# Kernel tuning notes

Hardware: AMD Instinct MI355X
Metric: run time of the kernel (lower is better)

The kernel has to match this reference:

```python
import jax, jax.numpy as jnp
import numpy as np

TOP_K = 2
SMOOTHING = 0.9


def setup_inputs() -> dict:
    key = jax.random.key(0)
    k1, k2, k3 = jax.random.split(key, 3)
    T, D, E = 16384, 2048, 64
    x = jax.random.normal(k1, (T, D), dtype=jnp.float32)
    gate_w = jax.random.normal(k2, (D, E), dtype=jnp.float32) * (1.0 / np.sqrt(D))
    expert_loads = jax.random.uniform(k3, (E,), dtype=jnp.float32)
    expert_loads = expert_loads / jnp.sum(expert_loads)  # normalized load estimate
    return {"x": x, "gate_w": gate_w, "expert_loads": expert_loads}


def reference(x, gate_w, expert_loads):
    T, _ = x.shape
    E = gate_w.shape[1]
    # Gate projection: [T, D] @ [D, E] -> [T, E]
    logits = jnp.matmul(x, gate_w)
    # Load-balancing bias injection (ExpertLoadBalancer.get_balancing_biases):
    # bias = -(load - 1/E) * 2, added to logits for expert *selection* only.
    biases = -(expert_loads - 1.0 / E) * 2.0
    _, top_idx = jax.lax.top_k(logits + biases[None, :], TOP_K)  # [T, K] int32
    # Routing weights: softmax over the selected (unbiased) logits.
    top_logits = jnp.take_along_axis(logits, top_idx, axis=1)  # [T, K]
    routing_weights = jax.nn.softmax(top_logits, axis=-1)  # [T, K]
    # Vectorized load update (replaces the Python double loop in update_loads):
    # scatter-add routing weights per expert, normalize by token count, EMA-smooth.
    current_loads = jax.ops.segment_sum(
        routing_weights.reshape(-1), top_idx.reshape(-1), num_segments=E
    ) / T
    new_loads = SMOOTHING * expert_loads + (1.0 - SMOOTHING) * current_loads
    return routing_weights, top_idx, new_loads
```

## Files before the change

kernel.cpp:

```cpp
#include <hip/hip_runtime.h>

#define TT 16384
#define DD 2048
#define EE 64

typedef __attribute__((ext_vector_type(8))) short bf16x8;
typedef __attribute__((ext_vector_type(8))) unsigned short ushort8;
typedef __attribute__((ext_vector_type(4))) float f32x4;

__device__ __forceinline__ unsigned short bf16_rne(float f) {
    unsigned u = __float_as_uint(f);
    return (unsigned short)((u + 0x7FFFu + ((u >> 16) & 1u)) >> 16);
}
__device__ __forceinline__ float bf16_f32(unsigned short h) {
    return __uint_as_float(((unsigned)h) << 16);
}
__device__ __forceinline__ unsigned cvt_pk(float lo, float hi) {
    unsigned r;
    asm("v_cvt_pk_bf16_f32 %0, %1, %2" : "=v"(r) : "v"(lo), "v"(hi));
    return r;
}
__device__ __forceinline__ bf16x8 pack4(unsigned a, unsigned b, unsigned c, unsigned d) {
    union { unsigned u[4]; bf16x8 v; } t;
    t.u[0] = a; t.u[1] = b; t.u[2] = c; t.u[3] = d;
    return t.v;
}
__device__ __forceinline__ void gload16(void* lds, const void* g) {
    __builtin_amdgcn_global_load_lds(
        (const __attribute__((address_space(1))) unsigned int*)g,
        (__attribute__((address_space(3))) unsigned int*)lds, 16, 0, 0);
}

__global__ __launch_bounds__(256)
void wconv(const float* __restrict__ wg, unsigned short* __restrict__ wpack) {
    const int t = (int)blockIdx.x * 256 + threadIdx.x;
    const int K0 = t >> 9, h = (t >> 8) & 1, m = (t >> 6) & 3, lane = t & 63;
    const int e = m * 16 + (lane & 15);
    const int ks = K0 * 32 + (lane >> 4) * 8;
    ushort8 v;
#pragma unroll
    for (int j = 0; j < 8; ++j) {
        const float f = wg[(size_t)(ks + j) * EE + e];
        const unsigned short hi = bf16_rne(f);
        v[j] = h ? bf16_rne(f - bf16_f32(hi)) : hi;
    }
    *(ushort8*)(wpack + ((size_t)(K0 * 8 + h * 4 + m) * 64 + lane) * 8) = v;
}

__global__ __launch_bounds__(512, 4)
void gate_fused(const float* __restrict__ x, const unsigned short* __restrict__ wpack,
                const float* __restrict__ loads, float* __restrict__ out,
                float* __restrict__ binpart) {
    __shared__ __align__(16) float arena[3 * 4096];
    __shared__ float bins[2][64];

    const int tid = threadIdx.x, lane = tid & 63, w = tid >> 6;
    const int tg = w >> 2, q = w & 3;
    const int tb = (int)blockIdx.x;

    f32x4 acc[4] = {{0,0,0,0},{0,0,0,0},{0,0,0,0},{0,0,0,0}};

    auto stage_x = [&](int s, float* rb) {
#pragma unroll
        for (int i = 0; i < 2; ++i) {
            const int n = (w << 1) | i;
            const int qw = n >> 2, g = n & 3;
            const int rowp = lane >> 3;
            const int row = g * 8 + rowp;
            const int c = (lane & 7) ^ rowp;
            gload16(rb + qw * 1024 + g * 256,
                    x + (size_t)(tb * 32 + row) * DD + qw * 512 + s * 32 + c * 4);
        }
    };
    auto loadW = [&](int t, bf16x8 (&wh)[4], bf16x8 (&wl)[4]) {
        const unsigned short* base = wpack + (size_t)(q * 16 + t) * 4096 + lane * 8;
#pragma unroll
        for (int m = 0; m < 4; ++m) {
            wh[m] = *(const bf16x8*)(base + (size_t)m * 512);
            wl[m] = *(const bf16x8*)(base + (size_t)(4 + m) * 512);
        }
    };
    auto compute = [&](const float* rb, bf16x8 (&wh)[4], bf16x8 (&wl)[4]) {
        const float* xq = rb + q * 1024;
        const int row = tg * 16 + (lane & 15);
        const int kgc = (lane >> 4) << 1;
        const int sw = row & 7;
        const f32x4 va = *(const f32x4*)(xq + row * 32 + ((kgc) ^ sw) * 4);
        const f32x4 vb = *(const f32x4*)(xq + row * 32 + ((kgc + 1) ^ sw) * 4);
        const float cf[8] = {va.x, va.y, va.z, va.w, vb.x, vb.y, vb.z, vb.w};
        unsigned ph[4], pl[4];
#pragma unroll
        for (int j = 0; j < 4; ++j) {
            ph[j] = cvt_pk(cf[2 * j], cf[2 * j + 1]);
            const float h0 = __uint_as_float(ph[j] << 16);
            const float h1 = __uint_as_float(ph[j] & 0xFFFF0000u);
            pl[j] = cvt_pk(cf[2 * j] - h0, cf[2 * j + 1] - h1);
        }
        const bf16x8 bhi = pack4(ph[0], ph[1], ph[2], ph[3]);
        const bf16x8 blo = pack4(pl[0], pl[1], pl[2], pl[3]);
#pragma unroll
        for (int m = 0; m < 4; ++m) {
            acc[m] = __builtin_amdgcn_mfma_f32_16x16x32_bf16(wh[m], bhi, acc[m], 0, 0, 0);
            acc[m] = __builtin_amdgcn_mfma_f32_16x16x32_bf16(wh[m], blo, acc[m], 0, 0, 0);
            acc[m] = __builtin_amdgcn_mfma_f32_16x16x32_bf16(wl[m], bhi, acc[m], 0, 0, 0);
        }
    };

    float *p0 = arena, *p1 = arena + 4096, *p2 = arena + 8192;
    bf16x8 whA[4], wlA[4], whB[4], wlB[4];

    stage_x(0, p0);
    stage_x(1, p1);
    loadW(0, whA, wlA);
    asm volatile("s_waitcnt vmcnt(10)" ::: "memory");
    __builtin_amdgcn_s_barrier();

#pragma unroll 1
    for (int s = 0; s < 14; s += 2) {
        stage_x(s + 2, p2);
        loadW(s + 1, whB, wlB);
        compute(p0, whA, wlA);
        asm volatile("s_waitcnt vmcnt(10)" ::: "memory");
        __builtin_amdgcn_s_barrier();
        { float* t_ = p0; p0 = p1; p1 = p2; p2 = t_; }

        stage_x(s + 3, p2);
        loadW(s + 2, whA, wlA);
        compute(p0, whB, wlB);
        asm volatile("s_waitcnt vmcnt(10)" ::: "memory");
        __builtin_amdgcn_s_barrier();
        { float* t_ = p0; p0 = p1; p1 = p2; p2 = t_; }
    }
    loadW(15, whB, wlB);
    compute(p0, whA, wlA);
    asm volatile("s_waitcnt vmcnt(8)" ::: "memory");
    __builtin_amdgcn_s_barrier();
    compute(p1, whB, wlB);

    __syncthreads();
    float* accb = arena;
    if (q != 0) {
#pragma unroll
        for (int m = 0; m < 4; ++m)
            *(f32x4*)(accb + ((size_t)((q - 1) * 128 + tg * 64 + lane) * 20 + m * 4)) = acc[m];
    }
    __syncthreads();
    if (q != 0) return;

    f32x4 r[4];
#pragma unroll
    for (int m = 0; m < 4; ++m) {
        f32x4 s_ = acc[m];
#pragma unroll
        for (int qq = 0; qq < 3; ++qq) {
            const f32x4 t_ =
                *(const f32x4*)(accb + ((size_t)(qq * 128 + tg * 64 + lane) * 20 + m * 4));
            s_.x += t_.x; s_.y += t_.y; s_.z += t_.z; s_.w += t_.w;
        }
        r[m] = s_;
    }

    const int col = lane & 15;
    const int tok = tb * 32 + tg * 16 + col;
    const int erow = (lane >> 4) * 4;
    float v1 = -3.4e38f, u1 = 0.0f, v2 = -3.4e38f, u2 = 0.0f;
    int i1 = 0x7fffffff, i2 = 0x7fffffff;
#pragma unroll
    for (int m = 0; m < 4; ++m)
#pragma unroll
        for (int rr = 0; rr < 4; ++rr) {
            const int e = m * 16 + erow + rr;
            const float u = r[m][rr];
            const float b = u - (loads[e] - 0.015625f) * 2.0f;
            if ((b > v1) || (b == v1 && e < i1)) {
                v2 = v1; u2 = u1; i2 = i1;
                v1 = b;  u1 = u;  i1 = e;
            } else if ((b > v2) || (b == v2 && e < i2)) {
                v2 = b; u2 = u; i2 = e;
            }
        }
#pragma unroll
    for (int s = 0; s < 2; ++s) {
        const int mask = 16 << s;
        const float ov1 = __shfl_xor(v1, mask), ou1 = __shfl_xor(u1, mask);
        const float ov2 = __shfl_xor(v2, mask), ou2 = __shfl_xor(u2, mask);
        const int oi1 = __shfl_xor(i1, mask), oi2 = __shfl_xor(i2, mask);
        if ((ov1 > v1) || (ov1 == v1 && oi1 < i1)) {
            if ((v1 > ov2) || (v1 == ov2 && i1 < oi2)) { v2 = v1; u2 = u1; i2 = i1; }
            else                                        { v2 = ov2; u2 = ou2; i2 = oi2; }
            v1 = ov1; u1 = ou1; i1 = oi1;
        } else if ((ov1 > v2) || (ov1 == v2 && oi1 < i2)) {
            v2 = ov1; u2 = ou1; i2 = oi1;
        }
    }

    bins[tg][lane] = 0.0f;
    if (lane < 16) {
        const float mx = fmaxf(u1, u2);
        const float e1 = __expf(u1 - mx), e2 = __expf(u2 - mx);
        const float w1 = e1 / (e1 + e2), w2 = e2 / (e1 + e2);
        *(float2*)(out + 2 * tok) = make_float2(w1, w2);
        *(float2*)(out + 2 * TT + 2 * tok) = make_float2((float)i1, (float)i2);
        atomicAdd(&bins[tg][i1], w1);
        atomicAdd(&bins[tg][i2], w2);
    }
    binpart[(size_t)(tb * 2 + tg) * 64 + lane] = bins[tg][lane];
}

__global__ __launch_bounds__(256)
void finalize1(const float* __restrict__ binpart, float* __restrict__ binmid) {
    __shared__ float p[4][64];
    const int e = threadIdx.x & 63, sub = threadIdx.x >> 6;
    float s = 0.0f;
#pragma unroll 4
    for (int r = 0; r < 16; ++r)
        s += binpart[(size_t)(((int)blockIdx.x * 4 + sub) * 16 + r) * 64 + e];
    p[sub][e] = s;
    __syncthreads();
    if (sub == 0)
        binmid[(int)blockIdx.x * 64 + e] = ((p[0][e] + p[1][e]) + p[2][e]) + p[3][e];
}

__global__ __launch_bounds__(64)
void finalize2(const float* __restrict__ binmid, const float* __restrict__ loads,
               float* __restrict__ out) {
    const int e = threadIdx.x;
    float s = 0.0f;
#pragma unroll
    for (int j = 0; j < 16; ++j) s += binmid[j * 64 + e];
    out[4 * TT + e] = 0.9f * loads[e] + 0.1f * (s * (1.0f / 16384.0f));
}

extern "C" void kernel_launch(void* const* d_in, const int* in_sizes, int n_in,
                              void* d_out, int out_size, void* d_ws, size_t ws_size,
                              hipStream_t stream) {
    const float* x = (const float*)d_in[0];
    const float* wg = (const float*)d_in[1];
    const float* loads = (const float*)d_in[2];
    float* out = (float*)d_out;

    unsigned short* wpack = (unsigned short*)d_ws;
    float* binpart = (float*)(wpack + (size_t)64 * 8 * 64 * 8);
    float* binmid = binpart + 1024 * 64;

    hipLaunchKernelGGL(wconv, dim3(128), dim3(256), 0, stream, wg, wpack);
    hipLaunchKernelGGL(gate_fused, dim3(512), dim3(512), 0, stream,
                       x, wpack, loads, out, binpart);
    hipLaunchKernelGGL(finalize1, dim3(16), dim3(256), 0, stream, binpart, binmid);
    hipLaunchKernelGGL(finalize2, dim3(1), dim3(64), 0, stream, binmid, loads, out);
}
```

Measured before the change: 45.48 us.

## Switch gate GEMM to 32x32x16 MFMA with full-K split across waves

Restructures the gate projection to use 32x32x16 bf16 MFMA tiles, where each of the 8 waves owns all 32 tokens and a 256-wide K slice. The previous layout split waves into token groups and used 16x16x32 tiles. The x staging moves from triple to double buffering with larger stages (8 iterations instead of 16), and the weight pack layout is reordered to match the new fragment shape. The cross-wave reduction now sums 8 partials through LDS, and the binning and finalize stages are adjusted for one bin row per block. The intent is fewer MFMA instructions and fewer loop iterations and barriers per block. The cost is a larger LDS footprint, which may limit occupancy, and a longer serial reduction done by one wave.

```diff
diff --git a/kernel.cpp b/kernel.cpp
--- a/kernel.cpp
+++ b/kernel.cpp
@@ -7,6 +7,7 @@
 typedef __attribute__((ext_vector_type(8))) short bf16x8;
 typedef __attribute__((ext_vector_type(8))) unsigned short ushort8;
 typedef __attribute__((ext_vector_type(4))) float f32x4;
+typedef __attribute__((ext_vector_type(16))) float f32x16;
 
 __device__ __forceinline__ unsigned short bf16_rne(float f) {
     unsigned u = __float_as_uint(f);
@@ -33,10 +34,10 @@
 
 __global__ __launch_bounds__(256)
 void wconv(const float* __restrict__ wg, unsigned short* __restrict__ wpack) {
-    const int t = (int)blockIdx.x * 256 + threadIdx.x;
-    const int K0 = t >> 9, h = (t >> 8) & 1, m = (t >> 6) & 3, lane = t & 63;
-    const int e = m * 16 + (lane & 15);
-    const int ks = K0 * 32 + (lane >> 4) * 8;
+    const int g = (int)blockIdx.x * 256 + threadIdx.x;
+    const int t = g >> 8, m = (g >> 7) & 1, h = (g >> 6) & 1, lane = g & 63;
+    const int e = m * 32 + (lane & 31);
+    const int ks = t * 16 + (lane >> 5) * 8;
     ushort8 v;
 #pragma unroll
     for (int j = 0; j < 8; ++j) {
@@ -44,133 +45,131 @@
         const unsigned short hi = bf16_rne(f);
         v[j] = h ? bf16_rne(f - bf16_f32(hi)) : hi;
     }
-    *(ushort8*)(wpack + ((size_t)(K0 * 8 + h * 4 + m) * 64 + lane) * 8) = v;
+    *(ushort8*)(wpack + (size_t)g * 8) = v;
 }
 
 __global__ __launch_bounds__(512, 4)
 void gate_fused(const float* __restrict__ x, const unsigned short* __restrict__ wpack,
                 const float* __restrict__ loads, float* __restrict__ out,
                 float* __restrict__ binpart) {
-    __shared__ __align__(16) float arena[3 * 4096];
-    __shared__ float bins[2][64];
-
-    const int tid = threadIdx.x, lane = tid & 63, w = tid >> 6;
-    const int tg = w >> 2, q = w & 3;
+    __shared__ __align__(16) float arena[16384];
+    __shared__ float bins[64];
+
+    const int tid = threadIdx.x, lane = tid & 63, q = tid >> 6;
     const int tb = (int)blockIdx.x;
-
-    f32x4 acc[4] = {{0,0,0,0},{0,0,0,0},{0,0,0,0},{0,0,0,0}};
+    const int tok = lane & 31, hi5 = lane >> 5;
+
+    f32x16 acc[2];
+#pragma unroll
+    for (int m = 0; m < 2; ++m)
+#pragma unroll
+        for (int r = 0; r < 16; ++r) acc[m][r] = 0.0f;
 
     auto stage_x = [&](int s, float* rb) {
 #pragma unroll
-        for (int i = 0; i < 2; ++i) {
-            const int n = (w << 1) | i;
-            const int qw = n >> 2, g = n & 3;
-            const int rowp = lane >> 3;
-            const int row = g * 8 + rowp;
-            const int c = (lane & 7) ^ rowp;
-            gload16(rb + qw * 1024 + g * 256,
-                    x + (size_t)(tb * 32 + row) * DD + qw * 512 + s * 32 + c * 4);
+        for (int i = 0; i < 4; ++i) {
+            const int row = i * 8 + (lane >> 3);
+            const int c = (lane & 7) ^ (lane >> 3);
+            gload16(rb + q * 1024 + i * 256,
+                    x + (size_t)(tb * 32 + row) * DD + q * 256 + s * 32 + c * 4);
         }
     };
-    auto loadW = [&](int t, bf16x8 (&wh)[4], bf16x8 (&wl)[4]) {
-        const unsigned short* base = wpack + (size_t)(q * 16 + t) * 4096 + lane * 8;
-#pragma unroll
-        for (int m = 0; m < 4; ++m) {
-            wh[m] = *(const bf16x8*)(base + (size_t)m * 512);
-            wl[m] = *(const bf16x8*)(base + (size_t)(4 + m) * 512);
-        }
+    bf16x8 W[8];
+    auto loadW = [&](int s) {
+        const unsigned short* base =
+            wpack + (size_t)((q * 16 + s * 2) * 4) * 512 + lane * 8;
+#pragma unroll
+        for (int f = 0; f < 8; ++f)
+            W[f] = *(const bf16x8*)(base + (size_t)f * 512);
     };
-    auto compute = [&](const float* rb, bf16x8 (&wh)[4], bf16x8 (&wl)[4]) {
-        const float* xq = rb + q * 1024;
-        const int row = tg * 16 + (lane & 15);
-        const int kgc = (lane >> 4) << 1;
-        const int sw = row & 7;
-        const f32x4 va = *(const f32x4*)(xq + row * 32 + ((kgc) ^ sw) * 4);
-        const f32x4 vb = *(const f32x4*)(xq + row * 32 + ((kgc + 1) ^ sw) * 4);
-        const float cf[8] = {va.x, va.y, va.z, va.w, vb.x, vb.y, vb.z, vb.w};
-        unsigned ph[4], pl[4];
-#pragma unroll
-        for (int j = 0; j < 4; ++j) {
-            ph[j] = cvt_pk(cf[2 * j], cf[2 * j + 1]);
-            const float h0 = __uint_as_float(ph[j] << 16);
-            const float h1 = __uint_as_float(ph[j] & 0xFFFF0000u);
-            pl[j] = cvt_pk(cf[2 * j] - h0, cf[2 * j + 1] - h1);
-        }
-        const bf16x8 bhi = pack4(ph[0], ph[1], ph[2], ph[3]);
-        const bf16x8 blo = pack4(pl[0], pl[1], pl[2], pl[3]);
-#pragma unroll
-        for (int m = 0; m < 4; ++m) {
-            acc[m] = __builtin_amdgcn_mfma_f32_16x16x32_bf16(wh[m], bhi, acc[m], 0, 0, 0);
-            acc[m] = __builtin_amdgcn_mfma_f32_16x16x32_bf16(wh[m], blo, acc[m], 0, 0, 0);
-            acc[m] = __builtin_amdgcn_mfma_f32_16x16x32_bf16(wl[m], bhi, acc[m], 0, 0, 0);
+    auto compute = [&](const float* rb) {
+        const float* xq = rb + q * 1024 + tok * 32;
+        const int key = tok & 7;
+#pragma unroll
+        for (int ts = 0; ts < 2; ++ts) {
+            const int c0 = ts * 4 + hi5 * 2;
+            const f32x4 va = *(const f32x4*)(xq + ((c0) ^ key) * 4);
+            const f32x4 vb = *(const f32x4*)(xq + ((c0 + 1) ^ key) * 4);
+            const float cf[8] = {va.x, va.y, va.z, va.w, vb.x, vb.y, vb.z, vb.w};
+            unsigned ph[4], pl[4];
+#pragma unroll
+            for (int j = 0; j < 4; ++j) {
+                ph[j] = cvt_pk(cf[2 * j], cf[2 * j + 1]);
+                const float h0 = __uint_as_float(ph[j] << 16);
+                const float h1 = __uint_as_float(ph[j] & 0xFFFF0000u);
+                pl[j] = cvt_pk(cf[2 * j] - h0, cf[2 * j + 1] - h1);
+            }
+            const bf16x8 bhi = pack4(ph[0], ph[1], ph[2], ph[3]);
+            const bf16x8 blo = pack4(pl[0], pl[1], pl[2], pl[3]);
+#pragma unroll
+            for (int m = 0; m < 2; ++m) {
+                acc[m] = __builtin_amdgcn_mfma_f32_32x32x16_bf16(
+                    W[ts * 4 + m * 2], bhi, acc[m], 0, 0, 0);
+                acc[m] = __builtin_amdgcn_mfma_f32_32x32x16_bf16(
+                    W[ts * 4 + m * 2], blo, acc[m], 0, 0, 0);
+                acc[m] = __builtin_amdgcn_mfma_f32_32x32x16_bf16(
+                    W[ts * 4 + m * 2 + 1], bhi, acc[m], 0, 0, 0);
+            }
         }
     };
 
-    float *p0 = arena, *p1 = arena + 4096, *p2 = arena + 8192;
-    bf16x8 whA[4], wlA[4], whB[4], wlB[4];
-
-    stage_x(0, p0);
-    stage_x(1, p1);
-    loadW(0, whA, wlA);
-    asm volatile("s_waitcnt vmcnt(10)" ::: "memory");
+    stage_x(0, arena);
+    loadW(0);
+    stage_x(1, arena + 8192);
+    asm volatile("s_waitcnt vmcnt(12)" ::: "memory");
     __builtin_amdgcn_s_barrier();
 
 #pragma unroll 1
-    for (int s = 0; s < 14; s += 2) {
-        stage_x(s + 2, p2);
-        loadW(s + 1, whB, wlB);
-        compute(p0, whA, wlA);
-        asm volatile("s_waitcnt vmcnt(10)" ::: "memory");
+    for (int s = 0; s < 8; ++s) {
+        compute((s & 1) ? arena + 8192 : arena);
         __builtin_amdgcn_s_barrier();
-        { float* t_ = p0; p0 = p1; p1 = p2; p2 = t_; }
-
-        stage_x(s + 3, p2);
-        loadW(s + 2, whA, wlA);
-        compute(p0, whB, wlB);
-        asm volatile("s_waitcnt vmcnt(10)" ::: "memory");
-        __builtin_amdgcn_s_barrier();
-        { float* t_ = p0; p0 = p1; p1 = p2; p2 = t_; }
-    }
-    loadW(15, whB, wlB);
-    compute(p0, whA, wlA);
-    asm volatile("s_waitcnt vmcnt(8)" ::: "memory");
-    __builtin_amdgcn_s_barrier();
-    compute(p1, whB, wlB);
-
-    __syncthreads();
-    float* accb = arena;
+        if (s < 6) {
+            loadW(s + 1);
+            stage_x(s + 2, (s & 1) ? arena + 8192 : arena);
+            asm volatile("s_waitcnt vmcnt(12)" ::: "memory");
+            __builtin_amdgcn_s_barrier();
+        } else if (s == 6) {
+            loadW(7);
+            asm volatile("s_waitcnt vmcnt(8)" ::: "memory");
+            __builtin_amdgcn_s_barrier();
+        }
+    }
+
     if (q != 0) {
-#pragma unroll
-        for (int m = 0; m < 4; ++m)
-            *(f32x4*)(accb + ((size_t)((q - 1) * 128 + tg * 64 + lane) * 20 + m * 4)) = acc[m];
+        float* ov = arena + (size_t)(q - 1) * 2304 + lane * 36;
+#pragma unroll
+        for (int m = 0; m < 2; ++m)
+#pragma unroll
+            for (int p = 0; p < 4; ++p) {
+                const f32x4 t_ = {acc[m][p * 4], acc[m][p * 4 + 1],
+                                  acc[m][p * 4 + 2], acc[m][p * 4 + 3]};
+                *(f32x4*)(ov + m * 16 + p * 4) = t_;
+            }
     }
     __syncthreads();
     if (q != 0) return;
 
-    f32x4 r[4];
-#pragma unroll
-    for (int m = 0; m < 4; ++m) {
-        f32x4 s_ = acc[m];
-#pragma unroll
-        for (int qq = 0; qq < 3; ++qq) {
-            const f32x4 t_ =
-                *(const f32x4*)(accb + ((size_t)(qq * 128 + tg * 64 + lane) * 20 + m * 4));
-            s_.x += t_.x; s_.y += t_.y; s_.z += t_.z; s_.w += t_.w;
-        }
-        r[m] = s_;
-    }
-
-    const int col = lane & 15;
-    const int tok = tb * 32 + tg * 16 + col;
-    const int erow = (lane >> 4) * 4;
+#pragma unroll 1
+    for (int qq = 0; qq < 7; ++qq) {
+        const float* ov = arena + (size_t)qq * 2304 + lane * 36;
+#pragma unroll
+        for (int m = 0; m < 2; ++m)
+#pragma unroll
+            for (int p = 0; p < 4; ++p) {
+                const f32x4 t_ = *(const f32x4*)(ov + m * 16 + p * 4);
+#pragma unroll
+                for (int j = 0; j < 4; ++j) acc[m][p * 4 + j] += t_[j];
+            }
+    }
+
     float v1 = -3.4e38f, u1 = 0.0f, v2 = -3.4e38f, u2 = 0.0f;
     int i1 = 0x7fffffff, i2 = 0x7fffffff;
 #pragma unroll
-    for (int m = 0; m < 4; ++m)
-#pragma unroll
-        for (int rr = 0; rr < 4; ++rr) {
-            const int e = m * 16 + erow + rr;
-            const float u = r[m][rr];
+    for (int m = 0; m < 2; ++m)
+#pragma unroll
+        for (int r = 0; r < 16; ++r) {
+            const int e = m * 32 + (r & 3) + 8 * (r >> 2) + 4 * hi5;
+            const float u = acc[m][r];
             const float b = u - (loads[e] - 0.015625f) * 2.0f;
             if ((b > v1) || (b == v1 && e < i1)) {
                 v2 = v1; u2 = u1; i2 = i1;
@@ -179,12 +178,10 @@
                 v2 = b; u2 = u; i2 = e;
             }
         }
-#pragma unroll
-    for (int s = 0; s < 2; ++s) {
-        const int mask = 16 << s;
-        const float ov1 = __shfl_xor(v1, mask), ou1 = __shfl_xor(u1, mask);
-        const float ov2 = __shfl_xor(v2, mask), ou2 = __shfl_xor(u2, mask);
-        const int oi1 = __shfl_xor(i1, mask), oi2 = __shfl_xor(i2, mask);
+    {
+        const float ov1 = __shfl_xor(v1, 32), ou1 = __shfl_xor(u1, 32);
+        const float ov2 = __shfl_xor(v2, 32), ou2 = __shfl_xor(u2, 32);
+        const int oi1 = __shfl_xor(i1, 32), oi2 = __shfl_xor(i2, 32);
         if ((ov1 > v1) || (ov1 == v1 && oi1 < i1)) {
             if ((v1 > ov2) || (v1 == ov2 && i1 < oi2)) { v2 = v1; u2 = u1; i2 = i1; }
             else                                        { v2 = ov2; u2 = ou2; i2 = oi2; }
@@ -194,17 +191,18 @@
         }
     }
 
-    bins[tg][lane] = 0.0f;
-    if (lane < 16) {
+    bins[lane] = 0.0f;
+    if (lane < 32) {
+        const int tg = tb * 32 + tok;
         const float mx = fmaxf(u1, u2);
         const float e1 = __expf(u1 - mx), e2 = __expf(u2 - mx);
         const float w1 = e1 / (e1 + e2), w2 = e2 / (e1 + e2);
-        *(float2*)(out + 2 * tok) = make_float2(w1, w2);
-        *(float2*)(out + 2 * TT + 2 * tok) = make_float2((float)i1, (float)i2);
-        atomicAdd(&bins[tg][i1], w1);
-        atomicAdd(&bins[tg][i2], w2);
-    }
-    binpart[(size_t)(tb * 2 + tg) * 64 + lane] = bins[tg][lane];
+        *(float2*)(out + 2 * tg) = make_float2(w1, w2);
+        *(float2*)(out + 2 * TT + 2 * tg) = make_float2((float)i1, (float)i2);
+        atomicAdd(&bins[i1], w1);
+        atomicAdd(&bins[i2], w2);
+    }
+    binpart[(size_t)tb * 64 + lane] = bins[lane];
 }
 
 __global__ __launch_bounds__(256)
@@ -212,9 +210,9 @@
     __shared__ float p[4][64];
     const int e = threadIdx.x & 63, sub = threadIdx.x >> 6;
     float s = 0.0f;
-#pragma unroll 4
-    for (int r = 0; r < 16; ++r)
-        s += binpart[(size_t)(((int)blockIdx.x * 4 + sub) * 16 + r) * 64 + e];
+#pragma unroll
+    for (int r = 0; r < 8; ++r)
+        s += binpart[(size_t)(((int)blockIdx.x * 4 + sub) * 8 + r) * 64 + e];
     p[sub][e] = s;
     __syncthreads();
     if (sub == 0)
@@ -241,7 +239,7 @@
 
     unsigned short* wpack = (unsigned short*)d_ws;
     float* binpart = (float*)(wpack + (size_t)64 * 8 * 64 * 8);
-    float* binmid = binpart + 1024 * 64;
+    float* binmid = binpart + 512 * 64;
 
     hipLaunchKernelGGL(wconv, dim3(128), dim3(256), 0, stream, wg, wpack);
     hipLaunchKernelGGL(gate_fused, dim3(512), dim3(512), 0, stream,
```

After: 45.88 us. Within noise of the previous version (+0.9%).
